# Optimization experiments

Measured on AMD Instinct MI355X. Metric: run time of the kernel, lower is better.

The kernel has to match this reference:

```python
import jax, jax.numpy as jnp
import numpy as np

B, N = 8, 1024
C = [256, 512, 1024]
C2 = C[1]
KV = sum(C)            # 1792
H = 4                  # num_attention_heads
EXPAND = 4
LN_EPS = 1e-6
IN_EPS = 1e-5          # nn.InstanceNorm2d default eps


def setup_inputs() -> dict:
    key = jax.random.key(0)
    ks = jax.random.split(key, 16)
    s = 0.02
    inp = {
        "emb1": jax.random.normal(ks[0], (B, N, C[0]), jnp.float32),
        "emb2": jax.random.normal(ks[1], (B, N, C[1]), jnp.float32),
        "emb3": jax.random.normal(ks[2], (B, N, C[2]), jnp.float32),
        # per-head projection weights stored as [in, out] (torch Linear applies x @ W.T)
        "Wq": jax.random.normal(ks[3], (H, C2, C2), jnp.float32) * s,
        "Wk": jax.random.normal(ks[4], (H, KV, KV), jnp.float32) * s,
        "Wv": jax.random.normal(ks[5], (H, KV, KV), jnp.float32) * s,
        "Wout": jax.random.normal(ks[6], (C2, C2), jnp.float32) * s,
        "ln1_g": jnp.ones((C2,), jnp.float32),
        "ln1_b": jnp.zeros((C2,), jnp.float32),
        "lnall_g": jnp.ones((KV,), jnp.float32),
        "lnall_b": jnp.zeros((KV,), jnp.float32),
        "lnffn_g": jnp.ones((C2,), jnp.float32),
        "lnffn_b": jnp.zeros((C2,), jnp.float32),
        "fc1_w": jax.random.normal(ks[7], (C2, C2 * EXPAND), jnp.float32) * s,
        "fc1_b": jnp.zeros((C2 * EXPAND,), jnp.float32),
        "fc2_w": jax.random.normal(ks[8], (C2 * EXPAND, C2), jnp.float32) * s,
        "fc2_b": jnp.zeros((C2,), jnp.float32),
    }
    return inp


def _layer_norm(x, g, b, eps=LN_EPS):
    m = jnp.mean(x, axis=-1, keepdims=True)
    v = jnp.var(x, axis=-1, keepdims=True)
    return (x - m) * jax.lax.rsqrt(v + eps) * g + b


def _instance_norm2d(x, eps=IN_EPS):
    # x: [B, H, C2, KV]; normalize each (B,H) map over its last two dims (no affine)
    m = jnp.mean(x, axis=(-2, -1), keepdims=True)
    v = jnp.var(x, axis=(-2, -1), keepdims=True)
    return (x - m) * jax.lax.rsqrt(v + eps)


def reference(emb1, emb2, emb3, Wq, Wk, Wv, Wout,
              ln1_g, ln1_b, lnall_g, lnall_b, lnffn_g, lnffn_b,
              fc1_w, fc1_b, fc2_w, fc2_b):
    org2 = emb2
    emb_all = jnp.concatenate([emb1, emb2, emb3], axis=2)        # [B,N,KV]
    cx2 = _layer_norm(emb2, ln1_g, ln1_b)                         # [B,N,C2]
    emb_all = _layer_norm(emb_all, lnall_g, lnall_b)              # [B,N,KV]

    # batched per-head projections (replaces the Python ModuleList loop)
    q = jnp.einsum('bnc,hcd->bhnd', cx2, Wq)                      # [B,H,N,C2]
    k = jnp.einsum('bnc,hcd->bhnd', emb_all, Wk)                  # [B,H,N,KV]
    v = jnp.einsum('bnc,hcd->bhnd', emb_all, Wv)                  # [B,H,N,KV]

    # channel attention: q^T k over the token axis
    scores = jnp.einsum('bhnc,bhnk->bhck', q, k) / np.sqrt(KV)    # [B,H,C2,KV]
    probs = jax.nn.softmax(_instance_norm2d(scores), axis=3)      # [B,H,C2,KV]

    # context = probs @ v^T, then mean over heads (fused into one einsum)
    ctx = jnp.einsum('bhck,bhnk->bnc', probs, v) / H              # [B,N,C2]
    o = ctx @ Wout                                                # [B,N,C2]

    cx2 = org2 + o
    x2 = _layer_norm(cx2, lnffn_g, lnffn_b)
    x2 = jax.nn.gelu(x2 @ fc1_w + fc1_b, approximate=False)
    x2 = x2 @ fc2_w + fc2_b
    return x2 + cx2
```

## Files before the change

kernel.cpp:

```cpp
#include <hip/hip_runtime.h>
#include <cstdint>
#include <cmath>

typedef __bf16 bf16_t;
typedef __attribute__((ext_vector_type(8))) __bf16 bf16x8;
typedef __attribute__((ext_vector_type(4))) float f32x4;

#define AS_G(x) ((__attribute__((address_space(1))) void*)(x))
#define AS_L(x) ((__attribute__((address_space(3))) void*)(x))

#define BK 64

#define BSZ 8
#define NTOK 1024
#define CC2 512
#define KVD 1792
#define NH 4
#define FFD 2048
#define ROWS 8192

#define BARM()   asm volatile("s_barrier" ::: "memory")
#define VMCNT8() asm volatile("s_waitcnt vmcnt(8)" ::: "memory")
#define VMCNT0() asm volatile("s_waitcnt vmcnt(0)" ::: "memory")
#define LGKMD()  asm volatile("s_waitcnt lgkmcnt(0)" ::: "memory")


__device__ __forceinline__ void stage_pair(const bf16_t* __restrict__ A,
                                           const bf16_t* __restrict__ B,
                                           int ld, bf16_t* ldsA, bf16_t* ldsB, int tid)
{
#pragma unroll
  for (int it = 0; it < 4; ++it) {
    int chunk = it * 256 + tid;
    int r = chunk >> 3;
    int s = chunk & 7;
    int cg = ((s ^ (r & 7)) << 3);
    __builtin_amdgcn_global_load_lds(AS_G(A + (long)r * ld + cg),
                                     AS_L(ldsA + chunk * 8), 16, 0, 0);
    __builtin_amdgcn_global_load_lds(AS_G(B + (long)r * ld + cg),
                                     AS_L(ldsB + chunk * 8), 16, 0, 0);
  }
}

__device__ __forceinline__ void mfma_step(const bf16_t* ldsA, const bf16_t* ldsB,
                                          f32x4 acc[4][4], int wr, int wc, int lane, int kc)
{
  const int quad = lane >> 4, l16 = lane & 15;
  bf16x8 a[4], b[4];
#pragma unroll
  for (int i = 0; i < 4; ++i) {
    int r = wr * 64 + i * 16 + l16;
    int slot = (kc + quad) ^ (r & 7);
    a[i] = *(const bf16x8*)(ldsA + r * BK + slot * 8);
  }
#pragma unroll
  for (int j = 0; j < 4; ++j) {
    int r = wc * 64 + j * 16 + l16;
    int slot = (kc + quad) ^ (r & 7);
    b[j] = *(const bf16x8*)(ldsB + r * BK + slot * 8);
  }
#pragma unroll
  for (int i = 0; i < 4; ++i)
#pragma unroll
    for (int j = 0; j < 4; ++j)
      acc[i][j] = __builtin_amdgcn_mfma_f32_16x16x32_bf16(a[i], b[j], acc[i][j], 0, 0, 0);
}

#define GEMM_PROLOG() \
  __shared__ __align__(16) bf16_t ldsA[2][128 * BK]; \
  __shared__ __align__(16) bf16_t ldsB[2][128 * BK]; \
  const int tid = threadIdx.x; \
  const int wave = tid >> 6, lane = tid & 63; \
  const int wr = wave >> 1, wc = wave & 1; \
  f32x4 acc[4][4] = {};

#define GEMM_LOOP(Aptr, Bptr, Kdim) { \
  const bf16_t* Ap_ = (Aptr); const bf16_t* Bp_ = (Bptr); const int Kd_ = (Kdim); \
  const int nt_ = Kd_ / BK; \
  stage_pair(Ap_, Bp_, Kd_, ldsA[0], ldsB[0], tid); \
  for (int t = 0; t < nt_; ++t) { \
    const int cur = t & 1; \
    if (t + 1 < nt_) { \
      stage_pair(Ap_ + (t + 1) * BK, Bp_ + (t + 1) * BK, Kd_, ldsA[cur ^ 1], ldsB[cur ^ 1], tid); \
      VMCNT8(); \
    } else { VMCNT0(); } \
    BARM(); \
    mfma_step(ldsA[cur], ldsB[cur], acc, wr, wc, lane, 0); \
    mfma_step(ldsA[cur], ldsB[cur], acc, wr, wc, lane, 4); \
    LGKMD(); \
    BARM(); \
  } }

template <typename F>
__device__ __forceinline__ void epilogue_apply(f32x4 acc[4][4], int wr, int wc, int lane, F f)
{
  const int quad = lane >> 4, l16 = lane & 15;
#pragma unroll
  for (int i = 0; i < 4; ++i)
#pragma unroll
    for (int j = 0; j < 4; ++j)
#pragma unroll
      for (int r = 0; r < 4; ++r)
        f(wr * 64 + i * 16 + quad * 4 + r, wc * 64 + j * 16 + l16, acc[i][j][r]);
}


__device__ __forceinline__ void stage256(const bf16_t* __restrict__ A,
                                         const bf16_t* __restrict__ B,
                                         int ld, bf16_t* ldsA, bf16_t* ldsB, int tid)
{
#pragma unroll
  for (int it = 0; it < 4; ++it) {
    int chunk = it * 512 + tid;
    int r = chunk >> 3;
    int s = chunk & 7;
    int cg = ((s ^ (r & 7)) << 3);
    __builtin_amdgcn_global_load_lds(AS_G(A + (long)r * ld + cg),
                                     AS_L(ldsA + chunk * 8), 16, 0, 0);
    __builtin_amdgcn_global_load_lds(AS_G(B + (long)r * ld + cg),
                                     AS_L(ldsB + chunk * 8), 16, 0, 0);
  }
}

__device__ __forceinline__ void qread_a(const bf16_t* ldsOp, int wr, int rh, int lane,
                                        bf16x8 a[4][2])
{
  const int quad = lane >> 4, l16 = lane & 15;
#pragma unroll
  for (int mi = 0; mi < 4; ++mi)
#pragma unroll
    for (int kc = 0; kc < 2; ++kc) {
      int r = wr * 128 + rh * 64 + mi * 16 + l16;
      int slot = (kc * 4 + quad) ^ (r & 7);
      a[mi][kc] = *(const bf16x8*)(ldsOp + r * BK + slot * 8);
    }
}

__device__ __forceinline__ void qread_b(const bf16_t* ldsOp, int wc, int ch, int lane,
                                        bf16x8 b[2][2])
{
  const int quad = lane >> 4, l16 = lane & 15;
#pragma unroll
  for (int nj = 0; nj < 2; ++nj)
#pragma unroll
    for (int kc = 0; kc < 2; ++kc) {
      int r = wc * 64 + ch * 32 + nj * 16 + l16;
      int slot = (kc * 4 + quad) ^ (r & 7);
      b[nj][kc] = *(const bf16x8*)(ldsOp + r * BK + slot * 8);
    }
}

template <int RH, int CH>
__device__ __forceinline__ void mfma16(f32x4 acc[8][4], const bf16x8 a[4][2],
                                       const bf16x8 (&b)[2][2])
{
#pragma unroll
  for (int mi = 0; mi < 4; ++mi)
#pragma unroll
    for (int nj = 0; nj < 2; ++nj)
#pragma unroll
      for (int kc = 0; kc < 2; ++kc)
        acc[RH * 4 + mi][CH * 2 + nj] =
            __builtin_amdgcn_mfma_f32_16x16x32_bf16(a[mi][kc], b[nj][kc],
                                                    acc[RH * 4 + mi][CH * 2 + nj], 0, 0, 0);
}

#define GEMM256_PROLOG() \
  __shared__ __align__(16) bf16_t ldsA[2][256 * BK]; \
  __shared__ __align__(16) bf16_t ldsB[2][256 * BK]; \
  __shared__ float sred[16]; \
  (void)sred; \
  const int tid = threadIdx.x; \
  const int wave = tid >> 6, lane = tid & 63; \
  const int wr = wave >> 2, wc = wave & 3; \
  f32x4 acc[8][4] = {};

#define GEMM256_LOOP(Aptr, Bptr, Kdim) { \
  const bf16_t* Ap = (Aptr); const bf16_t* Bp = (Bptr); const int Kd = (Kdim); \
  const int nt = Kd / BK; \
  stage256(Ap, Bp, Kd, ldsA[0], ldsB[0], tid); \
  for (int t = 0; t < nt; ++t) { \
    const int cur = t & 1; \
    if (t + 1 < nt) { \
      stage256(Ap + (t + 1) * BK, Bp + (t + 1) * BK, Kd, ldsA[cur ^ 1], ldsB[cur ^ 1], tid); \
      VMCNT8(); \
    } else { VMCNT0(); } \
    BARM(); \
    { \
      bf16x8 a[4][2], b0[2][2], b1[2][2]; \
      qread_a(ldsA[cur], wr, 0, lane, a); \
      qread_b(ldsB[cur], wc, 0, lane, b0); \
      qread_b(ldsB[cur], wc, 1, lane, b1); \
      mfma16<0, 0>(acc, a, b0); \
      mfma16<0, 1>(acc, a, b1); \
      qread_a(ldsA[cur], wr, 1, lane, a); \
      mfma16<1, 0>(acc, a, b0); \
      mfma16<1, 1>(acc, a, b1); \
    } \
    LGKMD(); \
    BARM(); \
  } }

template <typename F>
__device__ __forceinline__ void epi256(f32x4 acc[8][4], int wr, int wc, int lane, F f)
{
  const int quad = lane >> 4, l16 = lane & 15;
#pragma unroll
  for (int i = 0; i < 8; ++i)
#pragma unroll
    for (int j = 0; j < 4; ++j)
#pragma unroll
      for (int r = 0; r < 4; ++r)
        f(wr * 128 + (i >> 2) * 64 + (i & 3) * 16 + quad * 4 + r,
          wc * 64 + (j >> 1) * 32 + (j & 1) * 16 + l16, acc[i][j][r]);
}

__device__ __forceinline__ void swz224(int& bx, int& by, int& bz)
{
  int lid = blockIdx.x + 2 * (blockIdx.y + 7 * blockIdx.z);
  int xcd = lid & 7, s = lid >> 3;
  int hh = xcd >> 2, bp = xcd & 3;
  int y = s % 7, t2 = s / 7;
  bx = t2 & 1;
  by = y;
  bz = hh * 8 + bp * 2 + (t2 >> 1);
}


__global__ void zstats_k(float* s)
{
  if (threadIdx.x < 64) s[threadIdx.x] = 0.f;
}

__global__ __launch_bounds__(256) void tconv_k(const float* __restrict__ in,
                                               bf16_t* __restrict__ out, int R, int Cc)
{
  __shared__ float tile[32][33];
  const long base = (long)blockIdx.z * R * Cc;
  const int c0 = blockIdx.x * 32, r0 = blockIdx.y * 32;
  const int tx = threadIdx.x & 31, ty = threadIdx.x >> 5;
#pragma unroll
  for (int i = 0; i < 4; ++i)
    tile[ty + i * 8][tx] = in[base + (long)(r0 + ty + i * 8) * Cc + c0 + tx];
  __syncthreads();
#pragma unroll
  for (int i = 0; i < 4; ++i)
    out[base + (long)(c0 + ty + i * 8) * R + r0 + tx] = (bf16_t)tile[tx][ty + i * 8];
}

__global__ __launch_bounds__(256) void tconv_bf_k(const bf16_t* __restrict__ in,
                                                  bf16_t* __restrict__ out, int R, int Cc)
{
  __shared__ float tile[32][33];
  const long base = (long)blockIdx.z * R * Cc;
  const int c0 = blockIdx.x * 32, r0 = blockIdx.y * 32;
  const int tx = threadIdx.x & 31, ty = threadIdx.x >> 5;
#pragma unroll
  for (int i = 0; i < 4; ++i)
    tile[ty + i * 8][tx] = (float)in[base + (long)(r0 + ty + i * 8) * Cc + c0 + tx];
  __syncthreads();
#pragma unroll
  for (int i = 0; i < 4; ++i)
    out[base + (long)(c0 + ty + i * 8) * R + r0 + tx] = (bf16_t)tile[tx][ty + i * 8];
}

__global__ __launch_bounds__(256) void cast_k(const float* __restrict__ in,
                                              bf16_t* __restrict__ out, long n)
{
  long i = ((long)blockIdx.x * 256 + threadIdx.x) * 4;
  if (i + 3 < n) {
    float4 v = *(const float4*)(in + i);
    out[i] = (bf16_t)v.x; out[i + 1] = (bf16_t)v.y;
    out[i + 2] = (bf16_t)v.z; out[i + 3] = (bf16_t)v.w;
  }
}

__global__ __launch_bounds__(256) void msum_add_k(const bf16_t* __restrict__ M,
                                                  bf16_t* __restrict__ O)
{
  long i = ((long)blockIdx.x * 256 + threadIdx.x) * 8;
  bf16x8 x = *(const bf16x8*)(M + i);
  bf16x8 y = *(const bf16x8*)(M + (long)8 * CC2 * KVD + i);
  bf16x8 r;
#pragma unroll
  for (int j = 0; j < 8; ++j) r[j] = (bf16_t)((float)x[j] + (float)y[j]);
  *(bf16x8*)(O + i) = r;
}

__global__ __launch_bounds__(256) void ln_concat_k(const float* __restrict__ e1,
                                                   const float* __restrict__ e2,
                                                   const float* __restrict__ e3,
                                                   const float* __restrict__ g1,
                                                   const float* __restrict__ b1,
                                                   const float* __restrict__ ga,
                                                   const float* __restrict__ ba,
                                                   bf16_t* __restrict__ cxln,
                                                   bf16_t* __restrict__ embln)
{
  const long row = blockIdx.x;
  const float* p1 = e1 + row * 256;
  const float* p2 = e2 + row * 512;
  const float* p3 = e3 + row * 1024;
  const int t = threadIdx.x;
  float vals[7];
  float sa = 0.f, qa = 0.f;
#pragma unroll
  for (int i = 0; i < 7; ++i) {
    int idx = t + i * 256;
    float x = (idx < 256) ? p1[idx] : (idx < 768 ? p2[idx - 256] : p3[idx - 768]);
    vals[i] = x;
    sa += x; qa += x * x;
  }
  float s2 = vals[1] + vals[2];
  float q2 = vals[1] * vals[1] + vals[2] * vals[2];
  for (int off = 32; off; off >>= 1) {
    sa += __shfl_down(sa, off, 64); qa += __shfl_down(qa, off, 64);
    s2 += __shfl_down(s2, off, 64); q2 += __shfl_down(q2, off, 64);
  }
  __shared__ float red[4][4];
  const int wave = t >> 6, lane = t & 63;
  if (lane == 0) { red[0][wave] = sa; red[1][wave] = qa; red[2][wave] = s2; red[3][wave] = q2; }
  __syncthreads();
  float SA = red[0][0] + red[0][1] + red[0][2] + red[0][3];
  float QA = red[1][0] + red[1][1] + red[1][2] + red[1][3];
  float S2 = red[2][0] + red[2][1] + red[2][2] + red[2][3];
  float Q2 = red[3][0] + red[3][1] + red[3][2] + red[3][3];
  float ma = SA * (1.f / 1792.f);
  float va = QA * (1.f / 1792.f) - ma * ma;
  float rsa = rsqrtf(va + 1e-6f);
  float m2 = S2 * (1.f / 512.f);
  float v2 = Q2 * (1.f / 512.f) - m2 * m2;
  float rs2 = rsqrtf(v2 + 1e-6f);
#pragma unroll
  for (int i = 0; i < 7; ++i) {
    int idx = t + i * 256;
    embln[row * 1792 + idx] = (bf16_t)((vals[i] - ma) * rsa * ga[idx] + ba[idx]);
  }
  cxln[row * 512 + t]       = (bf16_t)((vals[1] - m2) * rs2 * g1[t] + b1[t]);
  cxln[row * 512 + t + 256] = (bf16_t)((vals[2] - m2) * rs2 * g1[t + 256] + b1[t + 256]);
}

__global__ __launch_bounds__(256) void ln2_k(const float* __restrict__ X,
                                             const float* __restrict__ g,
                                             const float* __restrict__ bb,
                                             bf16_t* __restrict__ Y)
{
  const long row = blockIdx.x;
  const float* p = X + row * 512;
  const int t = threadIdx.x;
  float x0 = p[t], x1 = p[t + 256];
  float s = x0 + x1, q = x0 * x0 + x1 * x1;
  for (int off = 32; off; off >>= 1) {
    s += __shfl_down(s, off, 64); q += __shfl_down(q, off, 64);
  }
  __shared__ float red[2][4];
  const int wave = t >> 6, lane = t & 63;
  if (lane == 0) { red[0][wave] = s; red[1][wave] = q; }
  __syncthreads();
  float S = red[0][0] + red[0][1] + red[0][2] + red[0][3];
  float Q = red[1][0] + red[1][1] + red[1][2] + red[1][3];
  float m = S * (1.f / 512.f);
  float v = Q * (1.f / 512.f) - m * m;
  float rs = rsqrtf(v + 1e-6f);
  Y[row * 512 + t]       = (bf16_t)((x0 - m) * rs * g[t] + bb[t]);
  Y[row * 512 + t + 256] = (bf16_t)((x1 - m) * rs * g[t + 256] + bb[t + 256]);
}

__global__ __launch_bounds__(256) void softmax_k(bf16_t* __restrict__ SC,
                                                 const float* __restrict__ stats)
{
  const long rowid = blockIdx.x;
  const int z = (int)(rowid >> 9);
  const float inv_cnt = 1.f / (512.f * 1792.f);
  float m = stats[2 * z] * inv_cnt;
  float var = stats[2 * z + 1] * inv_cnt - m * m;
  float rs = rsqrtf(var + 1e-5f);
  bf16_t* rowp = SC + rowid * 1792;
  const int t = threadIdx.x;
  float v[7];
  float mx = -1e30f;
#pragma unroll
  for (int i = 0; i < 7; ++i) {
    v[i] = (float)rowp[t + i * 256] * rs;
    mx = fmaxf(mx, v[i]);
  }
  for (int off = 32; off; off >>= 1) mx = fmaxf(mx, __shfl_down(mx, off, 64));
  __shared__ float red[8];
  const int wave = t >> 6, lane = t & 63;
  if (lane == 0) red[wave] = mx;
  __syncthreads();
  mx = fmaxf(fmaxf(red[0], red[1]), fmaxf(red[2], red[3]));
  float sum = 0.f;
#pragma unroll
  for (int i = 0; i < 7; ++i) { v[i] = __expf(v[i] - mx); sum += v[i]; }
  for (int off = 32; off; off >>= 1) sum += __shfl_down(sum, off, 64);
  if (lane == 0) red[4 + wave] = sum;
  __syncthreads();
  float inv = 1.f / (red[4] + red[5] + red[6] + red[7]);
#pragma unroll
  for (int i = 0; i < 7; ++i) rowp[t + i * 256] = (bf16_t)(v[i] * inv);
}


__global__ __launch_bounds__(256) void gemm_ab(const bf16_t* __restrict__ A, long astride,
                                               const bf16_t* __restrict__ B, long bstride,
                                               bf16_t* __restrict__ C, long cstride,
                                               int K, int ldc)
{
  const int z = blockIdx.z;
  GEMM_PROLOG();
  const bf16_t* Ap = A + z * astride + (long)blockIdx.x * 128 * K;
  const bf16_t* Bp = B + z * bstride + (long)blockIdx.y * 128 * K;
  GEMM_LOOP(Ap, Bp, K);
  bf16_t* Cb = C + (long)z * cstride;
  const int rbase = blockIdx.x * 128, cbase = blockIdx.y * 128;
  epilogue_apply(acc, wr, wc, lane, [&](int rr, int cc, float v) {
    Cb[(long)(rbase + rr) * ldc + cbase + cc] = (bf16_t)v;
  });
}

__global__ __launch_bounds__(512, 2) void gemm_t1_256(const bf16_t* __restrict__ WqT,
                                                      const bf16_t* __restrict__ Gt,
                                                      bf16_t* __restrict__ T1)
{
  int bxx, byy, bzz;
  swz224(bxx, byy, bzz);
  const int z = bzz, hh = z >> 3, b = z & 7;
  GEMM256_PROLOG();
  const bf16_t* Ap0 = WqT + (long)hh * CC2 * CC2 + (long)bxx * 256 * CC2;
  const bf16_t* Bp0 = Gt + (long)b * KVD * CC2 + (long)byy * 256 * CC2;
  GEMM256_LOOP(Ap0, Bp0, CC2);
  bf16_t* Cb = T1 + (long)z * CC2 * KVD;
  const int rbase = bxx * 256, cbase = byy * 256;
  epi256(acc, wr, wc, lane, [&](int rr, int cc, float v) {
    Cb[(long)(rbase + rr) * KVD + cbase + cc] = (bf16_t)v;
  });
}

__global__ __launch_bounds__(512, 2) void gemm_scores_256(const bf16_t* __restrict__ T1,
                                                          const bf16_t* __restrict__ WkT,
                                                          bf16_t* __restrict__ SC,
                                                          float* __restrict__ stats)
{
  int bxx, byy, bzz;
  swz224(bxx, byy, bzz);
  const int z = bzz, hh = z >> 3;
  GEMM256_PROLOG();
  const bf16_t* Ap0 = T1 + (long)z * CC2 * KVD + (long)bxx * 256 * KVD;
  const bf16_t* Bp0 = WkT + (long)hh * KVD * KVD + (long)byy * 256 * KVD;
  GEMM256_LOOP(Ap0, Bp0, KVD);
  const float scale = 0.02362277854f;
  bf16_t* Cb = SC + (long)z * CC2 * KVD;
  const int rbase = bxx * 256, cbase = byy * 256;
  float s = 0.f, q = 0.f;
  epi256(acc, wr, wc, lane, [&](int rr, int cc, float v) {
    v *= scale;
    Cb[(long)(rbase + rr) * KVD + cbase + cc] = (bf16_t)v;
    s += v; q += v * v;
  });
  for (int off = 32; off; off >>= 1) { s += __shfl_down(s, off, 64); q += __shfl_down(q, off, 64); }
  if (lane == 0) { sred[wave] = s; sred[8 + wave] = q; }
  __syncthreads();
  if (tid == 0) {
    float S = 0.f, Q = 0.f;
#pragma unroll
    for (int w = 0; w < 8; ++w) { S += sred[w]; Q += sred[8 + w]; }
    atomicAdd(&stats[2 * z], S);
    atomicAdd(&stats[2 * z + 1], Q);
  }
}

__global__ __launch_bounds__(512, 2) void gemm_macc_256(const bf16_t* __restrict__ P,
                                                        const bf16_t* __restrict__ WvB,
                                                        bf16_t* __restrict__ M, int first)
{
  int bxx, byy, bzz;
  swz224(bxx, byy, bzz);
  const int z = bzz, hh = z >> 3;
  GEMM256_PROLOG();
  const bf16_t* Ap0 = P + (long)z * CC2 * KVD + (long)bxx * 256 * KVD;
  const bf16_t* Bp0 = WvB + (long)hh * KVD * KVD + (long)byy * 256 * KVD;
  GEMM256_LOOP(Ap0, Bp0, KVD);
  bf16_t* Cb = M + (long)z * CC2 * KVD;
  const int rbase = bxx * 256, cbase = byy * 256;
  epi256(acc, wr, wc, lane, [&](int rr, int cc, float v) {
    long idx = (long)(rbase + rr) * KVD + cbase + cc;
    float prev = first ? 0.f : (float)Cb[idx];
    Cb[idx] = (bf16_t)(prev + v * 0.25f);
  });
}

__global__ __launch_bounds__(256) void gemm_ctx(const bf16_t* __restrict__ E,
                                                const bf16_t* __restrict__ Msum8,
                                                bf16_t* __restrict__ CTX)
{
  const int b = blockIdx.z;
  GEMM_PROLOG();
  const bf16_t* Ap = E + (long)b * NTOK * KVD + (long)blockIdx.x * 128 * KVD;
  const bf16_t* Bp = Msum8 + (long)b * CC2 * KVD + (long)blockIdx.y * 128 * KVD;
  GEMM_LOOP(Ap, Bp, KVD);
  bf16_t* Cb = CTX + (long)b * NTOK * CC2;
  const int rbase = blockIdx.x * 128, cbase = blockIdx.y * 128;
  epilogue_apply(acc, wr, wc, lane, [&](int rr, int cc, float v) {
    Cb[(long)(rbase + rr) * CC2 + cbase + cc] = (bf16_t)v;
  });
}

__global__ __launch_bounds__(256) void gemm_resid(const bf16_t* __restrict__ A,
                                                  const bf16_t* __restrict__ B,
                                                  const float* __restrict__ emb2,
                                                  float* __restrict__ CX2)
{
  GEMM_PROLOG();
  const bf16_t* Ap = A + (long)blockIdx.x * 128 * CC2;
  const bf16_t* Bp = B + (long)blockIdx.y * 128 * CC2;
  GEMM_LOOP(Ap, Bp, CC2);
  const int rbase = blockIdx.x * 128, cbase = blockIdx.y * 128;
  epilogue_apply(acc, wr, wc, lane, [&](int rr, int cc, float v) {
    long idx = (long)(rbase + rr) * CC2 + cbase + cc;
    CX2[idx] = v + emb2[idx];
  });
}

__global__ __launch_bounds__(512, 2) void gemm_gelu_256(const bf16_t* __restrict__ A,
                                                        const bf16_t* __restrict__ B,
                                                        const float* __restrict__ bias,
                                                        bf16_t* __restrict__ H)
{
  GEMM256_PROLOG();
  const bf16_t* Ap0 = A + (long)blockIdx.x * 256 * CC2;
  const bf16_t* Bp0 = B + (long)blockIdx.y * 256 * CC2;
  GEMM256_LOOP(Ap0, Bp0, CC2);
  const int rbase = blockIdx.x * 256, cbase = blockIdx.y * 256;
  epi256(acc, wr, wc, lane, [&](int rr, int cc, float v) {
    float x = v + bias[cbase + cc];
    float g = 0.5f * x * (1.0f + erff(x * 0.70710678118f));
    H[(long)(rbase + rr) * FFD + cbase + cc] = (bf16_t)g;
  });
}

__global__ __launch_bounds__(256) void gemm_out(const bf16_t* __restrict__ A,
                                                const bf16_t* __restrict__ B,
                                                const float* __restrict__ bias,
                                                const float* __restrict__ CX2,
                                                float* __restrict__ OUT)
{
  GEMM_PROLOG();
  const bf16_t* Ap = A + (long)blockIdx.x * 128 * FFD;
  const bf16_t* Bp = B + (long)blockIdx.y * 128 * FFD;
  GEMM_LOOP(Ap, Bp, FFD);
  const int rbase = blockIdx.x * 128, cbase = blockIdx.y * 128;
  epilogue_apply(acc, wr, wc, lane, [&](int rr, int cc, float v) {
    long idx = (long)(rbase + rr) * CC2 + cbase + cc;
    OUT[idx] = v + bias[cbase + cc] + CX2[idx];
  });
}


extern "C" void kernel_launch(void* const* d_in, const int* in_sizes, int n_in,
                              void* d_out, int out_size, void* d_ws, size_t ws_size,
                              hipStream_t stream)
{
  const float* emb1   = (const float*)d_in[0];
  const float* emb2   = (const float*)d_in[1];
  const float* emb3   = (const float*)d_in[2];
  const float* Wq     = (const float*)d_in[3];
  const float* Wk     = (const float*)d_in[4];
  const float* Wv     = (const float*)d_in[5];
  const float* Wout   = (const float*)d_in[6];
  const float* ln1_g  = (const float*)d_in[7];
  const float* ln1_b  = (const float*)d_in[8];
  const float* lnall_g = (const float*)d_in[9];
  const float* lnall_b = (const float*)d_in[10];
  const float* lnffn_g = (const float*)d_in[11];
  const float* lnffn_b = (const float*)d_in[12];
  const float* fc1_w  = (const float*)d_in[13];
  const float* fc1_b  = (const float*)d_in[14];
  const float* fc2_w  = (const float*)d_in[15];
  const float* fc2_b  = (const float*)d_in[16];
  float* out = (float*)d_out;

  char* ws = (char*)d_ws;
  size_t off = 0;
  auto alloc = [&](size_t bytes) {
    size_t r = off;
    off = (off + bytes + 255) & ~(size_t)255;
    return r;
  };

  size_t oEMBLN = alloc((size_t)ROWS * KVD * 2);
  size_t oCXLN  = alloc((size_t)ROWS * CC2 * 2);
  size_t oCX2   = alloc((size_t)ROWS * CC2 * 4);
  size_t oGt    = alloc((size_t)BSZ * KVD * CC2 * 2);
  size_t oMsum  = alloc((size_t)16 * CC2 * KVD * 2);
  size_t oWOT   = alloc((size_t)CC2 * CC2 * 2);
  size_t oF1T   = alloc((size_t)FFD * CC2 * 2);
  size_t oF2T   = alloc((size_t)CC2 * FFD * 2);
  size_t oSTATS = alloc(64 * 4);
  size_t oSCR   = alloc(0);
  size_t oCXLNT  = alloc((size_t)BSZ * CC2 * NTOK * 2);
  size_t oEMBLNT = alloc((size_t)BSZ * KVD * NTOK * 2);
  (void)ws_size; (void)in_sizes; (void)n_in; (void)out_size;

  bf16_t* EMBLN  = (bf16_t*)(ws + oEMBLN);
  bf16_t* CXLN   = (bf16_t*)(ws + oCXLN);
  float*  CX2    = (float*)(ws + oCX2);
  bf16_t* Gt     = (bf16_t*)(ws + oGt);
  bf16_t* Msum   = (bf16_t*)(ws + oMsum);
  bf16_t* WOT    = (bf16_t*)(ws + oWOT);
  bf16_t* F1T    = (bf16_t*)(ws + oF1T);
  bf16_t* F2T    = (bf16_t*)(ws + oF2T);
  float*  STATS  = (float*)(ws + oSTATS);
  bf16_t* CXLNT  = (bf16_t*)(ws + oCXLNT);
  bf16_t* EMBLNT = (bf16_t*)(ws + oEMBLNT);
  char* scr = ws + oSCR;
  auto rnd = [](size_t v) { return (v + 255) & ~(size_t)255; };
  bf16_t* WqT = (bf16_t*)(scr);
  bf16_t* WkT = (bf16_t*)(scr + rnd((size_t)2 * CC2 * CC2 * 2));
  bf16_t* WvB = (bf16_t*)((char*)WkT + rnd((size_t)2 * KVD * KVD * 2));
  bf16_t* T1  = (bf16_t*)((char*)WvB + rnd((size_t)2 * KVD * KVD * 2));
  bf16_t* SC  = (bf16_t*)((char*)T1 + rnd((size_t)16 * CC2 * KVD * 2));
  bf16_t* Msum8 = (bf16_t*)(scr);
  bf16_t* CTX   = (bf16_t*)(scr + rnd((size_t)8 * CC2 * KVD * 2));
  bf16_t* FFNH  = (bf16_t*)((char*)CTX + rnd((size_t)ROWS * CC2 * 2));
  bf16_t* X2LN = CXLN;

  zstats_k<<<1, 64, 0, stream>>>(STATS);
  tconv_k<<<dim3(16, 16), 256, 0, stream>>>(Wout, WOT, 512, 512);
  tconv_k<<<dim3(64, 16), 256, 0, stream>>>(fc1_w, F1T, 512, 2048);
  tconv_k<<<dim3(16, 64), 256, 0, stream>>>(fc2_w, F2T, 2048, 512);

  ln_concat_k<<<8192, 256, 0, stream>>>(emb1, emb2, emb3, ln1_g, ln1_b,
                                        lnall_g, lnall_b, CXLN, EMBLN);

  tconv_bf_k<<<dim3(16, 32, 8), 256, 0, stream>>>(CXLN, CXLNT, 1024, 512);
  tconv_bf_k<<<dim3(56, 32, 8), 256, 0, stream>>>(EMBLN, EMBLNT, 1024, 1792);
  gemm_ab<<<dim3(14, 4, 8), 256, 0, stream>>>(EMBLNT, (long)KVD * NTOK,
                                              CXLNT, (long)CC2 * NTOK,
                                              Gt, (long)KVD * CC2, NTOK, CC2);

  for (int g = 0; g < 2; ++g) {
    tconv_k<<<dim3(16, 16, 2), 256, 0, stream>>>(Wq + (long)g * 2 * CC2 * CC2, WqT, 512, 512);
    tconv_k<<<dim3(56, 56, 2), 256, 0, stream>>>(Wk + (long)g * 2 * KVD * KVD, WkT, 1792, 1792);
    cast_k<<<6272, 256, 0, stream>>>(Wv + (long)g * 2 * KVD * KVD, WvB, (long)2 * KVD * KVD);

    gemm_t1_256<<<dim3(2, 7, 16), 512, 0, stream>>>(WqT, Gt, T1);
    gemm_scores_256<<<dim3(2, 7, 16), 512, 0, stream>>>(T1, WkT, SC, STATS + g * 32);
    softmax_k<<<8192, 256, 0, stream>>>(SC, STATS + g * 32);
    gemm_macc_256<<<dim3(2, 7, 16), 512, 0, stream>>>(SC, WvB, Msum, g == 0 ? 1 : 0);
  }

  msum_add_k<<<3584, 256, 0, stream>>>(Msum, Msum8);
  gemm_ctx<<<dim3(8, 4, 8), 256, 0, stream>>>(EMBLN, Msum8, CTX);

  gemm_resid<<<dim3(64, 4), 256, 0, stream>>>(CTX, WOT, emb2, CX2);

  ln2_k<<<8192, 256, 0, stream>>>(CX2, lnffn_g, lnffn_b, X2LN);
  gemm_gelu_256<<<dim3(32, 8), 512, 0, stream>>>(X2LN, F1T, fc1_b, FFNH);
  gemm_out<<<dim3(64, 4), 256, 0, stream>>>(FFNH, F2T, fc2_b, CX2, out);
}
```

Baseline: 750.8 us.

## Merge head groups into single launches and split LDS staging across MFMA phases

```diff
diff --git a/kernel.cpp b/kernel.cpp
--- a/kernel.cpp
+++ b/kernel.cpp
@@ -21,6 +21,7 @@
 
 #define BARM()   asm volatile("s_barrier" ::: "memory")
 #define VMCNT8() asm volatile("s_waitcnt vmcnt(8)" ::: "memory")
+#define VMCNT4() asm volatile("s_waitcnt vmcnt(4)" ::: "memory")
 #define VMCNT0() asm volatile("s_waitcnt vmcnt(0)" ::: "memory")
 #define LGKMD()  asm volatile("s_waitcnt lgkmcnt(0)" ::: "memory")
 
@@ -105,12 +106,13 @@
 }
 
 
-__device__ __forceinline__ void stage256(const bf16_t* __restrict__ A,
-                                         const bf16_t* __restrict__ B,
-                                         int ld, bf16_t* ldsA, bf16_t* ldsB, int tid)
-{
-#pragma unroll
-  for (int it = 0; it < 4; ++it) {
+__device__ __forceinline__ void stage256h(const bf16_t* __restrict__ A,
+                                          const bf16_t* __restrict__ B,
+                                          int ld, bf16_t* ldsA, bf16_t* ldsB, int tid, int h)
+{
+#pragma unroll
+  for (int i = 0; i < 2; ++i) {
+    int it = h * 2 + i;
     int chunk = it * 512 + tid;
     int r = chunk >> 3;
     int s = chunk & 7;
@@ -178,12 +180,13 @@
 #define GEMM256_LOOP(Aptr, Bptr, Kdim) { \
   const bf16_t* Ap = (Aptr); const bf16_t* Bp = (Bptr); const int Kd = (Kdim); \
   const int nt = Kd / BK; \
-  stage256(Ap, Bp, Kd, ldsA[0], ldsB[0], tid); \
+  stage256h(Ap, Bp, Kd, ldsA[0], ldsB[0], tid, 0); \
+  stage256h(Ap, Bp, Kd, ldsA[0], ldsB[0], tid, 1); \
   for (int t = 0; t < nt; ++t) { \
     const int cur = t & 1; \
     if (t + 1 < nt) { \
-      stage256(Ap + (t + 1) * BK, Bp + (t + 1) * BK, Kd, ldsA[cur ^ 1], ldsB[cur ^ 1], tid); \
-      VMCNT8(); \
+      stage256h(Ap + (t + 1) * BK, Bp + (t + 1) * BK, Kd, ldsA[cur ^ 1], ldsB[cur ^ 1], tid, 0); \
+      VMCNT4(); \
     } else { VMCNT0(); } \
     BARM(); \
     { \
@@ -193,6 +196,8 @@
       qread_b(ldsB[cur], wc, 1, lane, b1); \
       mfma16<0, 0>(acc, a, b0); \
       mfma16<0, 1>(acc, a, b1); \
+      if (t + 1 < nt) \
+        stage256h(Ap + (t + 1) * BK, Bp + (t + 1) * BK, Kd, ldsA[cur ^ 1], ldsB[cur ^ 1], tid, 1); \
       qread_a(ldsA[cur], wr, 1, lane, a); \
       mfma16<1, 0>(acc, a, b0); \
       mfma16<1, 1>(acc, a, b1); \
@@ -215,15 +220,15 @@
           wc * 64 + (j >> 1) * 32 + (j & 1) * 16 + l16, acc[i][j][r]);
 }
 
-__device__ __forceinline__ void swz224(int& bx, int& by, int& bz)
+__device__ __forceinline__ void swzA(int mg, int& bx, int& by, int& bz)
 {
   int lid = blockIdx.x + 2 * (blockIdx.y + 7 * blockIdx.z);
   int xcd = lid & 7, s = lid >> 3;
-  int hh = xcd >> 2, bp = xcd & 3;
-  int y = s % 7, t2 = s / 7;
-  bx = t2 & 1;
+  int y = s % 7, t = s / 7;
+  bx = t & 1;
   by = y;
-  bz = hh * 8 + bp * 2 + (t2 >> 1);
+  if (mg) bz = (xcd >> 1) * 8 + (xcd & 1) * 4 + (t >> 1);
+  else    bz = (xcd >> 2) * 8 + (xcd & 3) * 2 + (t >> 1);
 }
 
 
@@ -276,14 +281,19 @@
 }
 
 __global__ __launch_bounds__(256) void msum_add_k(const bf16_t* __restrict__ M,
-                                                  bf16_t* __restrict__ O)
-{
+                                                  bf16_t* __restrict__ O, int nfold)
+{
+  const long SLICE = (long)8 * CC2 * KVD;
   long i = ((long)blockIdx.x * 256 + threadIdx.x) * 8;
-  bf16x8 x = *(const bf16x8*)(M + i);
-  bf16x8 y = *(const bf16x8*)(M + (long)8 * CC2 * KVD + i);
+  float acc[8] = {};
+  for (int h = 0; h < nfold; ++h) {
+    bf16x8 x = *(const bf16x8*)(M + h * SLICE + i);
+#pragma unroll
+    for (int j = 0; j < 8; ++j) acc[j] += (float)x[j];
+  }
   bf16x8 r;
 #pragma unroll
-  for (int j = 0; j < 8; ++j) r[j] = (bf16_t)((float)x[j] + (float)y[j]);
+  for (int j = 0; j < 8; ++j) r[j] = (bf16_t)acc[j];
   *(bf16x8*)(O + i) = r;
 }
 
@@ -421,10 +431,10 @@
 
 __global__ __launch_bounds__(512, 2) void gemm_t1_256(const bf16_t* __restrict__ WqT,
                                                       const bf16_t* __restrict__ Gt,
-                                                      bf16_t* __restrict__ T1)
+                                                      bf16_t* __restrict__ T1, int mg)
 {
   int bxx, byy, bzz;
-  swz224(bxx, byy, bzz);
+  swzA(mg, bxx, byy, bzz);
   const int z = bzz, hh = z >> 3, b = z & 7;
   GEMM256_PROLOG();
   const bf16_t* Ap0 = WqT + (long)hh * CC2 * CC2 + (long)bxx * 256 * CC2;
@@ -440,10 +450,10 @@
 __global__ __launch_bounds__(512, 2) void gemm_scores_256(const bf16_t* __restrict__ T1,
                                                           const bf16_t* __restrict__ WkT,
                                                           bf16_t* __restrict__ SC,
-                                                          float* __restrict__ stats)
+                                                          float* __restrict__ stats, int mg)
 {
   int bxx, byy, bzz;
-  swz224(bxx, byy, bzz);
+  swzA(mg, bxx, byy, bzz);
   const int z = bzz, hh = z >> 3;
   GEMM256_PROLOG();
   const bf16_t* Ap0 = T1 + (long)z * CC2 * KVD + (long)bxx * 256 * KVD;
@@ -472,10 +482,11 @@
 
 __global__ __launch_bounds__(512, 2) void gemm_macc_256(const bf16_t* __restrict__ P,
                                                         const bf16_t* __restrict__ WvB,
-                                                        bf16_t* __restrict__ M, int first)
+                                                        bf16_t* __restrict__ M,
+                                                        int first, int mg)
 {
   int bxx, byy, bzz;
-  swz224(bxx, byy, bzz);
+  swzA(mg, bxx, byy, bzz);
   const int z = bzz, hh = z >> 3;
   GEMM256_PROLOG();
   const bf16_t* Ap0 = P + (long)z * CC2 * KVD + (long)bxx * 256 * KVD;
@@ -579,6 +590,12 @@
   const float* fc2_w  = (const float*)d_in[15];
   const float* fc2_b  = (const float*)d_in[16];
   float* out = (float*)d_out;
+  (void)in_sizes; (void)n_in; (void)out_size;
+
+  const bool merged = ws_size >= (size_t)306 * 1000 * 1000;
+  const int nheads = merged ? 4 : 2;
+  const int nz = merged ? 32 : 16;
+  const int nmslot = merged ? 32 : 16;
 
   char* ws = (char*)d_ws;
   size_t off = 0;
@@ -592,7 +609,7 @@
   size_t oCXLN  = alloc((size_t)ROWS * CC2 * 2);
   size_t oCX2   = alloc((size_t)ROWS * CC2 * 4);
   size_t oGt    = alloc((size_t)BSZ * KVD * CC2 * 2);
-  size_t oMsum  = alloc((size_t)16 * CC2 * KVD * 2);
+  size_t oMsum  = alloc((size_t)nmslot * CC2 * KVD * 2);
   size_t oWOT   = alloc((size_t)CC2 * CC2 * 2);
   size_t oF1T   = alloc((size_t)FFD * CC2 * 2);
   size_t oF2T   = alloc((size_t)CC2 * FFD * 2);
@@ -600,7 +617,6 @@
   size_t oSCR   = alloc(0);
   size_t oCXLNT  = alloc((size_t)BSZ * CC2 * NTOK * 2);
   size_t oEMBLNT = alloc((size_t)BSZ * KVD * NTOK * 2);
-  (void)ws_size; (void)in_sizes; (void)n_in; (void)out_size;
 
   bf16_t* EMBLN  = (bf16_t*)(ws + oEMBLN);
   bf16_t* CXLN   = (bf16_t*)(ws + oCXLN);
@@ -613,13 +629,14 @@
   float*  STATS  = (float*)(ws + oSTATS);
   bf16_t* CXLNT  = (bf16_t*)(ws + oCXLNT);
   bf16_t* EMBLNT = (bf16_t*)(ws + oEMBLNT);
+
   char* scr = ws + oSCR;
   auto rnd = [](size_t v) { return (v + 255) & ~(size_t)255; };
   bf16_t* WqT = (bf16_t*)(scr);
-  bf16_t* WkT = (bf16_t*)(scr + rnd((size_t)2 * CC2 * CC2 * 2));
-  bf16_t* WvB = (bf16_t*)((char*)WkT + rnd((size_t)2 * KVD * KVD * 2));
-  bf16_t* T1  = (bf16_t*)((char*)WvB + rnd((size_t)2 * KVD * KVD * 2));
-  bf16_t* SC  = (bf16_t*)((char*)T1 + rnd((size_t)16 * CC2 * KVD * 2));
+  bf16_t* WkT = (bf16_t*)(scr + rnd((size_t)nheads * CC2 * CC2 * 2));
+  bf16_t* WvB = (bf16_t*)((char*)WkT + rnd((size_t)nheads * KVD * KVD * 2));
+  bf16_t* T1  = (bf16_t*)((char*)WvB + rnd((size_t)nheads * KVD * KVD * 2));
+  bf16_t* SC  = (bf16_t*)((char*)T1 + rnd((size_t)nz * CC2 * KVD * 2));
   bf16_t* Msum8 = (bf16_t*)(scr);
   bf16_t* CTX   = (bf16_t*)(scr + rnd((size_t)8 * CC2 * KVD * 2));
   bf16_t* FFNH  = (bf16_t*)((char*)CTX + rnd((size_t)ROWS * CC2 * 2));
@@ -639,18 +656,30 @@
                                               CXLNT, (long)CC2 * NTOK,
                                               Gt, (long)KVD * CC2, NTOK, CC2);
 
-  for (int g = 0; g < 2; ++g) {
-    tconv_k<<<dim3(16, 16, 2), 256, 0, stream>>>(Wq + (long)g * 2 * CC2 * CC2, WqT, 512, 512);
-    tconv_k<<<dim3(56, 56, 2), 256, 0, stream>>>(Wk + (long)g * 2 * KVD * KVD, WkT, 1792, 1792);
-    cast_k<<<6272, 256, 0, stream>>>(Wv + (long)g * 2 * KVD * KVD, WvB, (long)2 * KVD * KVD);
-
-    gemm_t1_256<<<dim3(2, 7, 16), 512, 0, stream>>>(WqT, Gt, T1);
-    gemm_scores_256<<<dim3(2, 7, 16), 512, 0, stream>>>(T1, WkT, SC, STATS + g * 32);
-    softmax_k<<<8192, 256, 0, stream>>>(SC, STATS + g * 32);
-    gemm_macc_256<<<dim3(2, 7, 16), 512, 0, stream>>>(SC, WvB, Msum, g == 0 ? 1 : 0);
-  }
-
-  msum_add_k<<<3584, 256, 0, stream>>>(Msum, Msum8);
+  if (merged) {
+    tconv_k<<<dim3(16, 16, 4), 256, 0, stream>>>(Wq, WqT, 512, 512);
+    tconv_k<<<dim3(56, 56, 4), 256, 0, stream>>>(Wk, WkT, 1792, 1792);
+    cast_k<<<12544, 256, 0, stream>>>(Wv, WvB, (long)4 * KVD * KVD);
+
+    gemm_t1_256<<<dim3(2, 7, 32), 512, 0, stream>>>(WqT, Gt, T1, 1);
+    gemm_scores_256<<<dim3(2, 7, 32), 512, 0, stream>>>(T1, WkT, SC, STATS, 1);
+    softmax_k<<<16384, 256, 0, stream>>>(SC, STATS);
+    gemm_macc_256<<<dim3(2, 7, 32), 512, 0, stream>>>(SC, WvB, Msum, 1, 1);
+    msum_add_k<<<3584, 256, 0, stream>>>(Msum, Msum8, 4);
+  } else {
+    for (int g = 0; g < 2; ++g) {
+      tconv_k<<<dim3(16, 16, 2), 256, 0, stream>>>(Wq + (long)g * 2 * CC2 * CC2, WqT, 512, 512);
+      tconv_k<<<dim3(56, 56, 2), 256, 0, stream>>>(Wk + (long)g * 2 * KVD * KVD, WkT, 1792, 1792);
+      cast_k<<<6272, 256, 0, stream>>>(Wv + (long)g * 2 * KVD * KVD, WvB, (long)2 * KVD * KVD);
+
+      gemm_t1_256<<<dim3(2, 7, 16), 512, 0, stream>>>(WqT, Gt, T1, 0);
+      gemm_scores_256<<<dim3(2, 7, 16), 512, 0, stream>>>(T1, WkT, SC, STATS + g * 32, 0);
+      softmax_k<<<8192, 256, 0, stream>>>(SC, STATS + g * 32);
+      gemm_macc_256<<<dim3(2, 7, 16), 512, 0, stream>>>(SC, WvB, Msum, g == 0 ? 1 : 0, 0);
+    }
+    msum_add_k<<<3584, 256, 0, stream>>>(Msum, Msum8, 2);
+  }
+
   gemm_ctx<<<dim3(8, 4, 8), 256, 0, stream>>>(EMBLN, Msum8, CTX);
 
   gemm_resid<<<dim3(64, 4), 256, 0, stream>>>(CTX, WOT, emb2, CX2);
```

After: 745.3 us (median of 2 runs). No clear change (-0.7%).
